# Performance work log

Hardware: AMD Instinct MI355X
Metric: run time of the kernel (lower is better)

The kernel has to match this reference:

```python
import jax, jax.numpy as jnp
import numpy as np

N = 50000
IN_CH = 256
HEADS = 8
OUT_CH = 32
E = 800000


def setup_inputs() -> dict:
    key = jax.random.key(0)
    k1, k2, k3, k4, k5 = jax.random.split(key, 5)
    x = jax.random.normal(k1, (N, IN_CH), dtype=jnp.float32)
    edge_index = jax.random.randint(k2, (2, E), 0, N, dtype=jnp.int64)
    # torch Linear(in, heads*out, bias=False): weight [heads*out, in]
    W = jax.random.normal(k3, (HEADS * OUT_CH, IN_CH), dtype=jnp.float32) / np.sqrt(IN_CH)
    # xavier_uniform over (1, heads, out)
    bound = float(np.sqrt(6.0 / (HEADS + OUT_CH)))
    attn_l = jax.random.uniform(k4, (1, HEADS, OUT_CH), minval=-bound, maxval=bound, dtype=jnp.float32)
    attn_r = jax.random.uniform(k5, (1, HEADS, OUT_CH), minval=-bound, maxval=bound, dtype=jnp.float32)
    return {"x": x, "edge_index": edge_index, "W": W, "attn_l": attn_l, "attn_r": attn_r}


def reference(x, edge_index, W, attn_l, attn_r):
    num_nodes = x.shape[0]
    # node-level projection: [N, H, C]
    xp = (x @ W.T).reshape(num_nodes, HEADS, OUT_CH).astype(jnp.float32)
    # add self loops
    loops = jnp.arange(num_nodes, dtype=edge_index.dtype)
    src = jnp.concatenate([edge_index[0], loops])
    dst = jnp.concatenate([edge_index[1], loops])
    # edge attention logits per head: [Etot, H]
    alpha_l = (xp * attn_l).sum(-1)[src]
    alpha_r = (xp * attn_r).sum(-1)[dst]
    alpha = jax.nn.leaky_relu(alpha_l + alpha_r, negative_slope=0.2)
    # global per-head max subtraction (as in the original), then scatter softmax over dst
    alpha = jnp.exp(alpha - alpha.max(axis=0, keepdims=True))
    alpha_sum = jax.ops.segment_sum(alpha, dst, num_segments=num_nodes)  # [N, H]
    alpha = alpha / jnp.maximum(alpha_sum[dst], 1e-6)
    # weighted aggregation: scatter-add alpha * x_src to dst, all heads at once
    msgs = alpha[:, :, None] * xp[src]  # [Etot, H, C]
    out = jax.ops.segment_sum(msgs, dst, num_segments=num_nodes)  # [N, H, C]
    return out.reshape(num_nodes, HEADS * OUT_CH)
```

## Files before the change

kernel.cpp:

```cpp
#include <hip/hip_runtime.h>
#include <math.h>

#define IN_CH   256
#define HEADS   8
#define OUT_CH  32
#define CAP     128

typedef __attribute__((ext_vector_type(8))) short s16x8;
typedef __attribute__((ext_vector_type(4))) float f32x4;

__device__ inline short f2bf(float f) {
  unsigned u = __builtin_bit_cast(unsigned, f);
  u += 0x7fffu + ((u >> 16) & 1u);
  return (short)(u >> 16);
}
__device__ inline float bf2f(unsigned short u) {
  unsigned v = ((unsigned)u) << 16;
  return __builtin_bit_cast(float, v);
}

__global__ __launch_bounds__(256) void prep(
    const float* __restrict__ W, short* __restrict__ Wb,
    int* __restrict__ cnt) {
  const int b = blockIdx.x;
  if (b < 64) {
    const int i = (b * 256 + (int)threadIdx.x) * 4;
    float4 v = *(const float4*)(W + i);
    ushort4 o;
    o.x = (unsigned short)f2bf(v.x);
    o.y = (unsigned short)f2bf(v.y);
    o.z = (unsigned short)f2bf(v.z);
    o.w = (unsigned short)f2bf(v.w);
    *(ushort4*)(Wb + i) = o;
  } else {
    const int i = ((b - 64) * 256 + (int)threadIdx.x) * 4;
    *(int4*)(cnt + i) = make_int4(0, 0, 0, 0);
  }
}

__global__ __launch_bounds__(256) void gemm_fill(
    const float* __restrict__ x, const short* __restrict__ Wb,
    const float* __restrict__ attn_l, const float* __restrict__ attn_r,
    short* __restrict__ xpb, float* __restrict__ al, float* __restrict__ ar,
    const int* __restrict__ src_idx, const int* __restrict__ dst_idx,
    int* __restrict__ cnt, int* __restrict__ csrs,
    int E, int n, int gemm_blocks) {
  if ((int)blockIdx.x >= gemm_blocks) {
    const int e = ((int)blockIdx.x - gemm_blocks) * 256 + (int)threadIdx.x;
    if (e < E + n) {
      int s, d;
      if (e < E) {
        s = src_idx[e];
        d = dst_idx[e];
      } else {
        s = d = e - E;
      }
      const int p = atomicAdd(&cnt[d], 1);
      if (p < CAP) csrs[d * CAP + p] = s;
    }
    return;
  }

  __shared__ short Ws[8 * 256 * 8];
  __shared__ short Xs[8 * 64 * 8];
  const int tid  = threadIdx.x;
  const int wave = tid >> 6;
  const int lane = tid & 63;
  const int nrow = lane & 15;
  const int kq   = lane >> 4;
  const int node0 = blockIdx.x * 64;

  f32x4 acc[4][4];
#pragma unroll
  for (int i = 0; i < 4; ++i)
#pragma unroll
    for (int j = 0; j < 4; ++j) acc[i][j] = (f32x4){0.f, 0.f, 0.f, 0.f};

  for (int k0 = 0; k0 < IN_CH; k0 += 64) {
    __syncthreads();
#pragma unroll
    for (int s = 0; s < 8; ++s) {
      s16x8 v = *(const s16x8*)(Wb + (size_t)tid * IN_CH + k0 + s * 8);
      *(s16x8*)&Ws[(s * 256 + tid) * 8] = v;
    }
#pragma unroll
    for (int p = 0; p < 2; ++p) {
      const int c = p * 256 + tid;
      const int row = c >> 3, o = c & 7;
      int grow = node0 + row;
      if (grow >= n) grow = n - 1;
      const float* xr = x + (size_t)grow * IN_CH + k0 + o * 8;
      float4 lo = *(const float4*)xr;
      float4 hi = *(const float4*)(xr + 4);
      s16x8 v;
      v[0] = f2bf(lo.x); v[1] = f2bf(lo.y); v[2] = f2bf(lo.z); v[3] = f2bf(lo.w);
      v[4] = f2bf(hi.x); v[5] = f2bf(hi.y); v[6] = f2bf(hi.z); v[7] = f2bf(hi.w);
      *(s16x8*)&Xs[(o * 64 + row) * 8] = v;
    }
    __syncthreads();
#pragma unroll
    for (int kk = 0; kk < 2; ++kk) {
      const int o = kk * 4 + kq;
      s16x8 af[4], bf[4];
#pragma unroll
      for (int i = 0; i < 4; ++i)
        af[i] = *(const s16x8*)&Ws[(o * 256 + wave * 64 + i * 16 + nrow) * 8];
#pragma unroll
      for (int j = 0; j < 4; ++j)
        bf[j] = *(const s16x8*)&Xs[(o * 64 + j * 16 + nrow) * 8];
#pragma unroll
      for (int i = 0; i < 4; ++i)
#pragma unroll
        for (int j = 0; j < 4; ++j)
          acc[i][j] = __builtin_amdgcn_mfma_f32_16x16x32_bf16(
              af[i], bf[j], acc[i][j], 0, 0, 0);
    }
  }

  float pl[4][2] = {}, pr[4][2] = {};
#pragma unroll
  for (int i = 0; i < 4; ++i) {
    const int oc = wave * 64 + i * 16 + kq * 4;
    const float4 la = *(const float4*)(attn_l + oc);
    const float4 ra = *(const float4*)(attn_r + oc);
    const int hh = i >> 1;
#pragma unroll
    for (int j = 0; j < 4; ++j) {
      const int node = node0 + j * 16 + nrow;
      ushort4 st;
      st.x = (unsigned short)f2bf(acc[i][j][0]);
      st.y = (unsigned short)f2bf(acc[i][j][1]);
      st.z = (unsigned short)f2bf(acc[i][j][2]);
      st.w = (unsigned short)f2bf(acc[i][j][3]);
      if (node < n) *(ushort4*)(xpb + (size_t)node * IN_CH + oc) = st;
      pl[j][hh] += acc[i][j][0] * la.x + acc[i][j][1] * la.y +
                   acc[i][j][2] * la.z + acc[i][j][3] * la.w;
      pr[j][hh] += acc[i][j][0] * ra.x + acc[i][j][1] * ra.y +
                   acc[i][j][2] * ra.z + acc[i][j][3] * ra.w;
    }
  }
#pragma unroll
  for (int j = 0; j < 4; ++j)
#pragma unroll
    for (int hh = 0; hh < 2; ++hh) {
      float vl = pl[j][hh], vr = pr[j][hh];
      vl += __shfl_xor(vl, 16); vl += __shfl_xor(vl, 32);
      vr += __shfl_xor(vr, 16); vr += __shfl_xor(vr, 32);
      const int node = node0 + j * 16 + nrow;
      if (kq == 0 && node < n) {
        al[node * HEADS + wave * 2 + hh] = vl;
        ar[node * HEADS + wave * 2 + hh] = vr;
      }
    }
}

__global__ __launch_bounds__(256) void gat_gather(
    const int* __restrict__ csrs, const int* __restrict__ cntp,
    const short* __restrict__ xpb, const float* __restrict__ al,
    const float* __restrict__ ar, float* __restrict__ out, int n) {
  const int gid = blockIdx.x * blockDim.x + threadIdx.x;
  const int d = gid >> 6;
  const int lane = gid & 63;
  if (d >= n) return;
  const int h = lane >> 3;
  const int start = d * CAP;
  int cnt = cntp[d];
  if (cnt > CAP) cnt = CAP;
  const float ard = ar[d * HEADS + h];

  f32x4 acc = {0.f, 0.f, 0.f, 0.f};
  float denom = 0.f;
  int j = 0;
  for (; j + 4 <= cnt; j += 4) {
    int s[4];
    ushort4 u[4];
    float wgt[4];
#pragma unroll
    for (int i = 0; i < 4; ++i) s[i] = csrs[start + j + i];
#pragma unroll
    for (int i = 0; i < 4; ++i)
      u[i] = *(const ushort4*)(xpb + (size_t)s[i] * IN_CH + lane * 4);
#pragma unroll
    for (int i = 0; i < 4; ++i) {
      float a = al[s[i] * HEADS + h] + ard;
      a = a > 0.f ? a : 0.2f * a;
      wgt[i] = __expf(a);
      denom += wgt[i];
    }
#pragma unroll
    for (int i = 0; i < 4; ++i) {
      acc[0] = fmaf(wgt[i], bf2f(u[i].x), acc[0]);
      acc[1] = fmaf(wgt[i], bf2f(u[i].y), acc[1]);
      acc[2] = fmaf(wgt[i], bf2f(u[i].z), acc[2]);
      acc[3] = fmaf(wgt[i], bf2f(u[i].w), acc[3]);
    }
  }
  for (; j < cnt; ++j) {
    const int s0 = csrs[start + j];
    const ushort4 u0 = *(const ushort4*)(xpb + (size_t)s0 * IN_CH + lane * 4);
    float a0 = al[s0 * HEADS + h] + ard;
    a0 = a0 > 0.f ? a0 : 0.2f * a0;
    const float w0 = __expf(a0);
    denom += w0;
    acc[0] = fmaf(w0, bf2f(u0.x), acc[0]);
    acc[1] = fmaf(w0, bf2f(u0.y), acc[1]);
    acc[2] = fmaf(w0, bf2f(u0.z), acc[2]);
    acc[3] = fmaf(w0, bf2f(u0.w), acc[3]);
  }
  const float inv = 1.f / fmaxf(denom, 1e-6f);
  acc *= inv;
  __builtin_nontemporal_store(acc,
      (f32x4*)(out + (size_t)d * IN_CH + lane * 4));
}

extern "C" void kernel_launch(void* const* d_in, const int* in_sizes, int n_in,
                              void* d_out, int out_size, void* d_ws,
                              size_t ws_size, hipStream_t stream) {
  const float* x      = (const float*)d_in[0];
  const int*   ei     = (const int*)d_in[1];
  const float* W      = (const float*)d_in[2];
  const float* attn_l = (const float*)d_in[3];
  const float* attn_r = (const float*)d_in[4];
  float* out = (float*)d_out;

  const int n = in_sizes[0] / IN_CH;
  const int E = in_sizes[1] / 2;
  const int Etot = E + n;

  short* xpb  = (short*)d_ws;
  short* Wb   = xpb + (size_t)n * IN_CH;
  float* al   = (float*)(Wb + IN_CH * IN_CH);
  float* ar   = al + (size_t)n * HEADS;
  int*   cnt  = (int*)(ar + (size_t)n * HEADS);
  int*   csrs = cnt + n;

  prep<<<113, 256, 0, stream>>>(W, Wb, cnt);

  const int gemm_blocks = (n + 63) / 64;
  const int fill_blocks = (Etot + 255) / 256;
  gemm_fill<<<gemm_blocks + fill_blocks, 256, 0, stream>>>(
      x, Wb, attn_l, attn_r, xpb, al, ar, ei, ei + E, cnt, csrs, E, n,
      gemm_blocks);

  const long long g_threads = (long long)n * 64;
  gat_gather<<<(int)((g_threads + 255) / 256), 256, 0, stream>>>(
      csrs, cnt, xpb, al, ar, out, n);
}
```

Baseline: 233.9 us.

## Drop W prep kernel, prefetch x tiles, widen fill and gather batching

Removes the separate prep kernel. W is now converted to bf16 inside each GEMM block, and the count array is zeroed with hipMemsetAsync. The x tile for the next k-step is prefetched into registers before the MFMA work, so global load latency can overlap with compute. Each fill block now handles four edges per thread, the gather loop processes eight neighbors per iteration for more memory-level parallelism, and launch bounds now request 4 blocks per SM. The cost is redundant W conversion in every GEMM block, with more fp32 W traffic, plus higher register pressure.

```diff
diff --git a/kernel.cpp b/kernel.cpp
--- a/kernel.cpp
+++ b/kernel.cpp
@@ -18,45 +18,36 @@
   unsigned v = ((unsigned)u) << 16;
   return __builtin_bit_cast(float, v);
 }
-
-__global__ __launch_bounds__(256) void prep(
-    const float* __restrict__ W, short* __restrict__ Wb,
-    int* __restrict__ cnt) {
-  const int b = blockIdx.x;
-  if (b < 64) {
-    const int i = (b * 256 + (int)threadIdx.x) * 4;
-    float4 v = *(const float4*)(W + i);
-    ushort4 o;
-    o.x = (unsigned short)f2bf(v.x);
-    o.y = (unsigned short)f2bf(v.y);
-    o.z = (unsigned short)f2bf(v.z);
-    o.w = (unsigned short)f2bf(v.w);
-    *(ushort4*)(Wb + i) = o;
-  } else {
-    const int i = ((b - 64) * 256 + (int)threadIdx.x) * 4;
-    *(int4*)(cnt + i) = make_int4(0, 0, 0, 0);
-  }
-}
-
-__global__ __launch_bounds__(256) void gemm_fill(
-    const float* __restrict__ x, const short* __restrict__ Wb,
+__device__ inline s16x8 cvt8(float4 lo, float4 hi) {
+  s16x8 v;
+  v[0] = f2bf(lo.x); v[1] = f2bf(lo.y); v[2] = f2bf(lo.z); v[3] = f2bf(lo.w);
+  v[4] = f2bf(hi.x); v[5] = f2bf(hi.y); v[6] = f2bf(hi.z); v[7] = f2bf(hi.w);
+  return v;
+}
+
+__global__ __launch_bounds__(256, 4) void gemm_fill(
+    const float* __restrict__ x, const float* __restrict__ Wf,
     const float* __restrict__ attn_l, const float* __restrict__ attn_r,
     short* __restrict__ xpb, float* __restrict__ al, float* __restrict__ ar,
     const int* __restrict__ src_idx, const int* __restrict__ dst_idx,
     int* __restrict__ cnt, int* __restrict__ csrs,
     int E, int n, int gemm_blocks) {
   if ((int)blockIdx.x >= gemm_blocks) {
-    const int e = ((int)blockIdx.x - gemm_blocks) * 256 + (int)threadIdx.x;
-    if (e < E + n) {
-      int s, d;
-      if (e < E) {
-        s = src_idx[e];
-        d = dst_idx[e];
-      } else {
-        s = d = e - E;
+    const int base = ((int)blockIdx.x - gemm_blocks) * 1024 + (int)threadIdx.x;
+#pragma unroll
+    for (int q = 0; q < 4; ++q) {
+      const int e = base + q * 256;
+      if (e < E + n) {
+        int s, d;
+        if (e < E) {
+          s = src_idx[e];
+          d = dst_idx[e];
+        } else {
+          s = d = e - E;
+        }
+        const int p = atomicAdd(&cnt[d], 1);
+        if (p < CAP) csrs[d * CAP + p] = s;
       }
-      const int p = atomicAdd(&cnt[d], 1);
-      if (p < CAP) csrs[d * CAP + p] = s;
     }
     return;
   }
@@ -70,6 +61,25 @@
   const int kq   = lane >> 4;
   const int node0 = blockIdx.x * 64;
 
+  int xrow[2], xoct[2];
+  const float* xbase[2];
+#pragma unroll
+  for (int p = 0; p < 2; ++p) {
+    const int c = p * 256 + tid;
+    xrow[p] = c >> 3;
+    xoct[p] = c & 7;
+    int grow = node0 + xrow[p];
+    if (grow >= n) grow = n - 1;
+    xbase[p] = x + (size_t)grow * IN_CH + xoct[p] * 8;
+  }
+
+  float4 xlo[2], xhi[2];
+#pragma unroll
+  for (int p = 0; p < 2; ++p) {
+    xlo[p] = *(const float4*)(xbase[p]);
+    xhi[p] = *(const float4*)(xbase[p] + 4);
+  }
+
   f32x4 acc[4][4];
 #pragma unroll
   for (int i = 0; i < 4; ++i)
@@ -80,22 +90,20 @@
     __syncthreads();
 #pragma unroll
     for (int s = 0; s < 8; ++s) {
-      s16x8 v = *(const s16x8*)(Wb + (size_t)tid * IN_CH + k0 + s * 8);
-      *(s16x8*)&Ws[(s * 256 + tid) * 8] = v;
-    }
-#pragma unroll
-    for (int p = 0; p < 2; ++p) {
-      const int c = p * 256 + tid;
-      const int row = c >> 3, o = c & 7;
-      int grow = node0 + row;
-      if (grow >= n) grow = n - 1;
-      const float* xr = x + (size_t)grow * IN_CH + k0 + o * 8;
-      float4 lo = *(const float4*)xr;
-      float4 hi = *(const float4*)(xr + 4);
-      s16x8 v;
-      v[0] = f2bf(lo.x); v[1] = f2bf(lo.y); v[2] = f2bf(lo.z); v[3] = f2bf(lo.w);
-      v[4] = f2bf(hi.x); v[5] = f2bf(hi.y); v[6] = f2bf(hi.z); v[7] = f2bf(hi.w);
-      *(s16x8*)&Xs[(o * 64 + row) * 8] = v;
+      const float* wr = Wf + (size_t)tid * IN_CH + k0 + s * 8;
+      float4 lo = *(const float4*)wr;
+      float4 hi = *(const float4*)(wr + 4);
+      *(s16x8*)&Ws[(s * 256 + tid) * 8] = cvt8(lo, hi);
+    }
+#pragma unroll
+    for (int p = 0; p < 2; ++p)
+      *(s16x8*)&Xs[(xoct[p] * 64 + xrow[p]) * 8] = cvt8(xlo[p], xhi[p]);
+    if (k0 + 64 < IN_CH) {
+#pragma unroll
+      for (int p = 0; p < 2; ++p) {
+        xlo[p] = *(const float4*)(xbase[p] + k0 + 64);
+        xhi[p] = *(const float4*)(xbase[p] + k0 + 64 + 4);
+      }
     }
     __syncthreads();
 #pragma unroll
@@ -171,6 +179,30 @@
   f32x4 acc = {0.f, 0.f, 0.f, 0.f};
   float denom = 0.f;
   int j = 0;
+  for (; j + 8 <= cnt; j += 8) {
+    int s[8];
+    ushort4 u[8];
+    float wgt[8];
+#pragma unroll
+    for (int i = 0; i < 8; ++i) s[i] = csrs[start + j + i];
+#pragma unroll
+    for (int i = 0; i < 8; ++i)
+      u[i] = *(const ushort4*)(xpb + (size_t)s[i] * IN_CH + lane * 4);
+#pragma unroll
+    for (int i = 0; i < 8; ++i) {
+      float a = al[s[i] * HEADS + h] + ard;
+      a = a > 0.f ? a : 0.2f * a;
+      wgt[i] = __expf(a);
+      denom += wgt[i];
+    }
+#pragma unroll
+    for (int i = 0; i < 8; ++i) {
+      acc[0] = fmaf(wgt[i], bf2f(u[i].x), acc[0]);
+      acc[1] = fmaf(wgt[i], bf2f(u[i].y), acc[1]);
+      acc[2] = fmaf(wgt[i], bf2f(u[i].z), acc[2]);
+      acc[3] = fmaf(wgt[i], bf2f(u[i].w), acc[3]);
+    }
+  }
   for (; j + 4 <= cnt; j += 4) {
     int s[4];
     ushort4 u[4];
@@ -228,18 +260,17 @@
   const int Etot = E + n;
 
   short* xpb  = (short*)d_ws;
-  short* Wb   = xpb + (size_t)n * IN_CH;
-  float* al   = (float*)(Wb + IN_CH * IN_CH);
+  float* al   = (float*)(xpb + (size_t)n * IN_CH);
   float* ar   = al + (size_t)n * HEADS;
   int*   cnt  = (int*)(ar + (size_t)n * HEADS);
   int*   csrs = cnt + n;
 
-  prep<<<113, 256, 0, stream>>>(W, Wb, cnt);
+  hipMemsetAsync(cnt, 0, (size_t)n * sizeof(int), stream);
 
   const int gemm_blocks = (n + 63) / 64;
-  const int fill_blocks = (Etot + 255) / 256;
+  const int fill_blocks = (Etot + 1023) / 1024;
   gemm_fill<<<gemm_blocks + fill_blocks, 256, 0, stream>>>(
-      x, Wb, attn_l, attn_r, xpb, al, ar, ei, ei + E, cnt, csrs, E, n,
+      x, W, attn_l, attn_r, xpb, al, ar, ei, ei + E, cnt, csrs, E, n,
       gemm_blocks);
 
   const long long g_threads = (long long)n * 64;
```

Result: slower. 241.7 us (+3.3%).
